# Kernel tuning notes

Measured on AMD Instinct MI355X. Metric: run time of the kernel, lower is better.

Reference implementation:

```python
import jax, jax.numpy as jnp
import numpy as np

IN_F = 8192
OUT_F = 8192
GROUP = 128
BATCH = 32


def dequantize(packed, scale, zero):
    """Unpack int4 pairs from uint8 and dequantize per 128-wide group.

    packed: [n_groups/2, 128] uint8 (hi nibble -> first half rows, lo nibble -> second half)
    scale, zero: [n_groups, 1] float32, broadcast over the 128 group columns.
    Returns dense weight [OUT_F, IN_F].
    """
    p = packed.astype(jnp.int32)
    hi = ((p >> 4) & 15).astype(jnp.float32)
    lo = (p & 15).astype(jnp.float32)
    w = jnp.concatenate([hi, lo], axis=0)          # [n_groups, 128]
    w = (w - zero) * scale                          # per-group affine dequant
    return w.reshape(OUT_F, IN_F)


def setup_inputs() -> dict:
    key = jax.random.key(0)
    k1, k2, k3, k4, k5 = jax.random.split(key, 5)
    n_groups = OUT_F * IN_F // GROUP
    x = jax.random.normal(k1, (BATCH, IN_F), dtype=jnp.float32)
    packed = jax.random.randint(k2, (n_groups // 2, GROUP), 0, 256, dtype=jnp.int32).astype(jnp.uint8)
    scale = jax.random.uniform(k3, (n_groups, 1), dtype=jnp.float32, minval=0.005, maxval=0.02)
    zero = jax.random.uniform(k4, (n_groups, 1), dtype=jnp.float32, minval=0.0, maxval=15.0)
    bias = jax.random.normal(k5, (OUT_F,), dtype=jnp.float32) * 0.01
    return {"x": x, "packed": packed, "scale": scale, "zero": zero, "bias": bias}


def reference(x, packed, scale, zero, bias):
    W = dequantize(packed, scale, zero)             # [OUT_F, IN_F]
    return x @ W.T + bias                            # [BATCH, OUT_F]
```

## Files before the change

### kernel.cpp

```cpp
#include <hip/hip_runtime.h>

#define IN_F 8192
#define OUT_F 8192
#define BATCH 32
#define HALFG ((OUT_F / 2) * (IN_F / 128))
#define NFRAG_HALF 16384

typedef _Float16 f16x2 __attribute__((ext_vector_type(2)));
typedef _Float16 f16x8 __attribute__((ext_vector_type(8)));
typedef float f32x4 __attribute__((ext_vector_type(4)));
typedef int i32x4 __attribute__((ext_vector_type(4)));

union AFrag { f16x8 v; i32x4 i4; };
union BFrag { f16x8 v; unsigned int u[4]; };
union F16x2U { f16x2 v; unsigned int u; };

__device__ inline f16x2 dq_pair(unsigned int h_bits, f16x2 s2, f16x2 zs2) {
    F16x2U h; h.u = h_bits;
    const f16x2 c1024 = {(_Float16)1024.0f, (_Float16)1024.0f};
    f16x2 n = h.v - c1024;
    return n * s2 + zs2;
}

__global__ __launch_bounds__(256) void xcvt_kernel(const float* __restrict__ x,
                                                   f16x8* __restrict__ xc) {
    int t = blockIdx.x * 256 + threadIdx.x;
    int r = t & 15;
    int q = (t >> 4) & 3;
    int k32 = (t >> 6) & 255;
    int half = t >> 14;
    int b = half * 16 + r;
    int kb = k32 * 32 + q * 4;
    float4 x0 = *(const float4*)(x + (size_t)b * IN_F + kb);
    float4 x1 = *(const float4*)(x + (size_t)b * IN_F + kb + 16);
    f16x8 o;
    o[0] = (_Float16)x0.x; o[1] = (_Float16)x0.y; o[2] = (_Float16)x0.z; o[3] = (_Float16)x0.w;
    o[4] = (_Float16)x1.x; o[5] = (_Float16)x1.y; o[6] = (_Float16)x1.z; o[7] = (_Float16)x1.w;
    xc[t] = o;
}

__global__ __launch_bounds__(256) void bias_init_kernel(const float4* __restrict__ bias,
                                                        float4* __restrict__ out) {
    int i = blockIdx.x * 256 + threadIdx.x;
    out[i] = bias[i & 2047];
}

template <int KSPLIT, bool FAST>
__global__ __launch_bounds__(256, 4) void qgemm_kernel(
    const float* __restrict__ xf, const f16x8* __restrict__ xc,
    const int* __restrict__ packed, const float* __restrict__ scale,
    const float* __restrict__ zero, float* __restrict__ outp) {
    constexpr int KCHUNK = IN_F / KSPLIT;
    constexpr int NKG = KCHUNK / 128;
    constexpr int NIT = NKG * 4;
    const int w = threadIdx.x >> 6;
    const int lane = threadIdx.x & 63;
    const int r = lane & 15;
    const int q = lane >> 4;
    const int nb = blockIdx.x;
    const int ks = blockIdx.y;
    const int pr = nb * 64 + w * 16 + r;
    const int kbase = ks * KCHUNK;

    f32x4 acc[2][2] = {{{0.f, 0.f, 0.f, 0.f}, {0.f, 0.f, 0.f, 0.f}},
                       {{0.f, 0.f, 0.f, 0.f}, {0.f, 0.f, 0.f, 0.f}}};

    const int* pk = packed + (size_t)pr * IN_F;

    const int ghi = pr * 64 + (kbase >> 7);
    float4 sh = *(const float4*)(scale + ghi);
    float4 zh = *(const float4*)(zero + ghi);
    float4 sl = *(const float4*)(scale + ghi + HALFG);
    float4 zl = *(const float4*)(zero + ghi + HALFG);
    const float sh_a[4] = {sh.x, sh.y, sh.z, sh.w};
    const float zh_a[4] = {zh.x, zh.y, zh.z, zh.w};
    const float sl_a[4] = {sl.x, sl.y, sl.z, sl.w};
    const float zl_a[4] = {zl.x, zl.y, zl.z, zl.w};
    f16x2 s2h[4], zs2h[4], s2l[4], zs2l[4];
#pragma unroll
    for (int kg = 0; kg < 4; ++kg) {
        _Float16 s = (_Float16)sh_a[kg];
        _Float16 zs = (_Float16)(-zh_a[kg] * sh_a[kg]);
        s2h[kg][0] = s; s2h[kg][1] = s; zs2h[kg][0] = zs; zs2h[kg][1] = zs;
        s = (_Float16)sl_a[kg];
        zs = (_Float16)(-zl_a[kg] * sl_a[kg]);
        s2l[kg][0] = s; s2l[kg][1] = s; zs2l[kg][0] = zs; zs2l[kg][1] = zs;
    }

#pragma unroll
    for (int it = 0; it < NIT; ++it) {
        const int kg = it >> 2;
        const int k0 = kbase + it * 32 + q * 4;
        i32x4 p0 = *(const i32x4*)(pk + k0);
        i32x4 p1 = *(const i32x4*)(pk + k0 + 16);
        AFrag a0, a1;
        if (FAST) {
            const int k32g = ks * NIT + it;
            a0.i4 = *(const i32x4*)(xc + (size_t)k32g * 64 + lane);
            a1.i4 = *(const i32x4*)(xc + (size_t)NFRAG_HALF + (size_t)k32g * 64 + lane);
        } else {
            float4 x00 = *(const float4*)(xf + (size_t)r * IN_F + k0);
            float4 x01 = *(const float4*)(xf + (size_t)r * IN_F + k0 + 16);
            float4 x10 = *(const float4*)(xf + (size_t)(16 + r) * IN_F + k0);
            float4 x11 = *(const float4*)(xf + (size_t)(16 + r) * IN_F + k0 + 16);
            a0.v[0] = (_Float16)x00.x; a0.v[1] = (_Float16)x00.y;
            a0.v[2] = (_Float16)x00.z; a0.v[3] = (_Float16)x00.w;
            a0.v[4] = (_Float16)x01.x; a0.v[5] = (_Float16)x01.y;
            a0.v[6] = (_Float16)x01.z; a0.v[7] = (_Float16)x01.w;
            a1.v[0] = (_Float16)x10.x; a1.v[1] = (_Float16)x10.y;
            a1.v[2] = (_Float16)x10.z; a1.v[3] = (_Float16)x10.w;
            a1.v[4] = (_Float16)x11.x; a1.v[5] = (_Float16)x11.y;
            a1.v[6] = (_Float16)x11.z; a1.v[7] = (_Float16)x11.w;
        }
        const unsigned int tt[4] = {
            (unsigned int)p0[0] | ((unsigned int)p0[1] << 16),
            (unsigned int)p0[2] | ((unsigned int)p0[3] << 16),
            (unsigned int)p1[0] | ((unsigned int)p1[1] << 16),
            (unsigned int)p1[2] | ((unsigned int)p1[3] << 16)};
        BFrag bhi, blo;
#pragma unroll
        for (int pi = 0; pi < 4; ++pi) {
            unsigned int hlo = (tt[pi] & 0x000F000Fu) | 0x64006400u;
            unsigned int hhi = ((tt[pi] >> 4) & 0x000F000Fu) | 0x64006400u;
            F16x2U wl, wh;
            wl.v = dq_pair(hlo, s2l[kg], zs2l[kg]);
            wh.v = dq_pair(hhi, s2h[kg], zs2h[kg]);
            blo.u[pi] = wl.u;
            bhi.u[pi] = wh.u;
        }
        acc[0][0] = __builtin_amdgcn_mfma_f32_16x16x32_f16(a0.v, bhi.v, acc[0][0], 0, 0, 0);
        acc[1][0] = __builtin_amdgcn_mfma_f32_16x16x32_f16(a1.v, bhi.v, acc[1][0], 0, 0, 0);
        acc[0][1] = __builtin_amdgcn_mfma_f32_16x16x32_f16(a0.v, blo.v, acc[0][1], 0, 0, 0);
        acc[1][1] = __builtin_amdgcn_mfma_f32_16x16x32_f16(a1.v, blo.v, acc[1][1], 0, 0, 0);
    }

#pragma unroll
    for (int bt = 0; bt < 2; ++bt) {
#pragma unroll
        for (int hl = 0; hl < 2; ++hl) {
            const int o = nb * 64 + w * 16 + r + hl * (OUT_F / 2);
#pragma unroll
            for (int j = 0; j < 4; ++j) {
                const int b = bt * 16 + q * 4 + j;
                if (FAST) {
                    outp[(size_t)ks * (BATCH * OUT_F) + (size_t)b * OUT_F + o] = acc[bt][hl][j];
                } else {
                    atomicAdd(&outp[(size_t)b * OUT_F + o], acc[bt][hl][j]);
                }
            }
        }
    }
}

template <int KSPLIT>
__global__ __launch_bounds__(256) void reduce_kernel(const float4* __restrict__ part,
                                                     const float4* __restrict__ bias,
                                                     float4* __restrict__ out) {
    int i = blockIdx.x * 256 + threadIdx.x;
    float4 s = bias[i & 2047];
#pragma unroll
    for (int k = 0; k < KSPLIT; ++k) {
        float4 p = part[(size_t)k * (BATCH * OUT_F / 4) + i];
        s.x += p.x; s.y += p.y; s.z += p.z; s.w += p.w;
    }
    out[i] = s;
}

extern "C" void kernel_launch(void* const* d_in, const int* in_sizes, int n_in,
                              void* d_out, int out_size, void* d_ws, size_t ws_size,
                              hipStream_t stream) {
    (void)in_sizes; (void)n_in; (void)out_size;
    const float* x = (const float*)d_in[0];
    const int* packed = (const int*)d_in[1];
    const float* scale = (const float*)d_in[2];
    const float* zero = (const float*)d_in[3];
    const float* bias = (const float*)d_in[4];
    float* out = (float*)d_out;

    constexpr int KSPLIT = 16;
    const size_t part_bytes = (size_t)KSPLIT * BATCH * OUT_F * sizeof(float);
    const size_t xc_bytes = (size_t)2 * NFRAG_HALF * 16;
    const size_t need = part_bytes + xc_bytes;

    if (ws_size >= need) {
        float* part = (float*)d_ws;
        f16x8* xc = (f16x8*)((char*)d_ws + part_bytes);
        xcvt_kernel<<<128, 256, 0, stream>>>(x, xc);
        qgemm_kernel<KSPLIT, true><<<dim3(OUT_F / 2 / 64, KSPLIT), 256, 0, stream>>>(
            nullptr, xc, packed, scale, zero, part);
        reduce_kernel<KSPLIT><<<256, 256, 0, stream>>>((const float4*)part,
                                                       (const float4*)bias, (float4*)out);
    } else {
        bias_init_kernel<<<256, 256, 0, stream>>>((const float4*)bias, (float4*)out);
        qgemm_kernel<KSPLIT, false><<<dim3(OUT_F / 2 / 64, KSPLIT), 256, 0, stream>>>(
            x, nullptr, packed, scale, zero, out);
    }
}
```

Before: 38.80 us.

## Store split-K partials as fp16 in transposed layout, double K-split, raise occupancy

```diff
diff --git a/kernel.cpp b/kernel.cpp
--- a/kernel.cpp
+++ b/kernel.cpp
@@ -7,6 +7,7 @@
 #define NFRAG_HALF 16384
 
 typedef _Float16 f16x2 __attribute__((ext_vector_type(2)));
+typedef _Float16 f16x4 __attribute__((ext_vector_type(4)));
 typedef _Float16 f16x8 __attribute__((ext_vector_type(8)));
 typedef float f32x4 __attribute__((ext_vector_type(4)));
 typedef int i32x4 __attribute__((ext_vector_type(4)));
@@ -14,6 +15,7 @@
 union AFrag { f16x8 v; i32x4 i4; };
 union BFrag { f16x8 v; unsigned int u[4]; };
 union F16x2U { f16x2 v; unsigned int u; };
+union F16x4U { f16x4 v; uint2 u2; };
 
 __device__ inline f16x2 dq_pair(unsigned int h_bits, f16x2 s2, f16x2 zs2) {
     F16x2U h; h.u = h_bits;
@@ -46,10 +48,10 @@
 }
 
 template <int KSPLIT, bool FAST>
-__global__ __launch_bounds__(256, 4) void qgemm_kernel(
+__global__ __launch_bounds__(256, 6) void qgemm_kernel(
     const float* __restrict__ xf, const f16x8* __restrict__ xc,
     const int* __restrict__ packed, const float* __restrict__ scale,
-    const float* __restrict__ zero, float* __restrict__ outp) {
+    const float* __restrict__ zero, void* __restrict__ outp) {
     constexpr int KCHUNK = IN_F / KSPLIT;
     constexpr int NKG = KCHUNK / 128;
     constexpr int NIT = NKG * 4;
@@ -68,17 +70,17 @@
     const int* pk = packed + (size_t)pr * IN_F;
 
     const int ghi = pr * 64 + (kbase >> 7);
-    float4 sh = *(const float4*)(scale + ghi);
-    float4 zh = *(const float4*)(zero + ghi);
-    float4 sl = *(const float4*)(scale + ghi + HALFG);
-    float4 zl = *(const float4*)(zero + ghi + HALFG);
-    const float sh_a[4] = {sh.x, sh.y, sh.z, sh.w};
-    const float zh_a[4] = {zh.x, zh.y, zh.z, zh.w};
-    const float sl_a[4] = {sl.x, sl.y, sl.z, sl.w};
-    const float zl_a[4] = {zl.x, zl.y, zl.z, zl.w};
-    f16x2 s2h[4], zs2h[4], s2l[4], zs2l[4];
-#pragma unroll
-    for (int kg = 0; kg < 4; ++kg) {
+    float2 sh = *(const float2*)(scale + ghi);
+    float2 zh = *(const float2*)(zero + ghi);
+    float2 sl = *(const float2*)(scale + ghi + HALFG);
+    float2 zl = *(const float2*)(zero + ghi + HALFG);
+    const float sh_a[2] = {sh.x, sh.y};
+    const float zh_a[2] = {zh.x, zh.y};
+    const float sl_a[2] = {sl.x, sl.y};
+    const float zl_a[2] = {zl.x, zl.y};
+    f16x2 s2h[2], zs2h[2], s2l[2], zs2l[2];
+#pragma unroll
+    for (int kg = 0; kg < NKG; ++kg) {
         _Float16 s = (_Float16)sh_a[kg];
         _Float16 zs = (_Float16)(-zh_a[kg] * sh_a[kg]);
         s2h[kg][0] = s; s2h[kg][1] = s; zs2h[kg][0] = zs; zs2h[kg][1] = zs;
@@ -139,13 +141,19 @@
 #pragma unroll
         for (int hl = 0; hl < 2; ++hl) {
             const int o = nb * 64 + w * 16 + r + hl * (OUT_F / 2);
-#pragma unroll
-            for (int j = 0; j < 4; ++j) {
-                const int b = bt * 16 + q * 4 + j;
-                if (FAST) {
-                    outp[(size_t)ks * (BATCH * OUT_F) + (size_t)b * OUT_F + o] = acc[bt][hl][j];
-                } else {
-                    atomicAdd(&outp[(size_t)b * OUT_F + o], acc[bt][hl][j]);
+            if (FAST) {
+                F16x4U pk4;
+                pk4.v[0] = (_Float16)acc[bt][hl][0];
+                pk4.v[1] = (_Float16)acc[bt][hl][1];
+                pk4.v[2] = (_Float16)acc[bt][hl][2];
+                pk4.v[3] = (_Float16)acc[bt][hl][3];
+                _Float16* part = (_Float16*)outp;
+                *(uint2*)(part + ((size_t)ks * OUT_F + o) * BATCH + bt * 16 + q * 4) = pk4.u2;
+            } else {
+#pragma unroll
+                for (int j = 0; j < 4; ++j) {
+                    const int b = bt * 16 + q * 4 + j;
+                    atomicAdd((float*)outp + (size_t)b * OUT_F + o, acc[bt][hl][j]);
                 }
             }
         }
@@ -153,17 +161,26 @@
 }
 
 template <int KSPLIT>
-__global__ __launch_bounds__(256) void reduce_kernel(const float4* __restrict__ part,
-                                                     const float4* __restrict__ bias,
-                                                     float4* __restrict__ out) {
-    int i = blockIdx.x * 256 + threadIdx.x;
-    float4 s = bias[i & 2047];
-#pragma unroll
-    for (int k = 0; k < KSPLIT; ++k) {
-        float4 p = part[(size_t)k * (BATCH * OUT_F / 4) + i];
-        s.x += p.x; s.y += p.y; s.z += p.z; s.w += p.w;
-    }
-    out[i] = s;
+__global__ __launch_bounds__(256) void reduce_kernel(const f16x8* __restrict__ part,
+                                                     const float* __restrict__ bias,
+                                                     float* __restrict__ out) {
+    const int o = blockIdx.x * 256 + threadIdx.x;
+    f16x8 s[4];
+#pragma unroll
+    for (int l = 0; l < 4; ++l) s[l] = part[(size_t)o * 4 + l];
+    for (int ks = 1; ks < KSPLIT; ++ks) {
+        const f16x8* p = part + ((size_t)ks * OUT_F + o) * 4;
+#pragma unroll
+        for (int l = 0; l < 4; ++l) s[l] += p[l];
+    }
+    const float bv = bias[o];
+#pragma unroll
+    for (int l = 0; l < 4; ++l) {
+#pragma unroll
+        for (int e = 0; e < 8; ++e) {
+            out[(size_t)(l * 8 + e) * OUT_F + o] = bv + (float)s[l][e];
+        }
+    }
 }
 
 extern "C" void kernel_launch(void* const* d_in, const int* in_sizes, int n_in,
@@ -177,19 +194,18 @@
     const float* bias = (const float*)d_in[4];
     float* out = (float*)d_out;
 
-    constexpr int KSPLIT = 16;
-    const size_t part_bytes = (size_t)KSPLIT * BATCH * OUT_F * sizeof(float);
+    constexpr int KSPLIT = 32;
+    const size_t part_bytes = (size_t)KSPLIT * BATCH * OUT_F * sizeof(_Float16);
     const size_t xc_bytes = (size_t)2 * NFRAG_HALF * 16;
     const size_t need = part_bytes + xc_bytes;
 
     if (ws_size >= need) {
-        float* part = (float*)d_ws;
+        _Float16* part = (_Float16*)d_ws;
         f16x8* xc = (f16x8*)((char*)d_ws + part_bytes);
         xcvt_kernel<<<128, 256, 0, stream>>>(x, xc);
         qgemm_kernel<KSPLIT, true><<<dim3(OUT_F / 2 / 64, KSPLIT), 256, 0, stream>>>(
             nullptr, xc, packed, scale, zero, part);
-        reduce_kernel<KSPLIT><<<256, 256, 0, stream>>>((const float4*)part,
-                                                       (const float4*)bias, (float4*)out);
+        reduce_kernel<KSPLIT><<<OUT_F / 256, 256, 0, stream>>>((const f16x8*)part, bias, out);
     } else {
         bias_init_kernel<<<256, 256, 0, stream>>>((const float4*)bias, (float4*)out);
         qgemm_kernel<KSPLIT, false><<<dim3(OUT_F / 2 / 64, KSPLIT), 256, 0, stream>>>(
```

After: 50.11 us. 1.29x slower.
